# Kernel tuning notes

Measured on AMD Instinct MI355X. Metric: run time of the kernel, lower is better.

The kernel has to match this reference:

```python
import jax, jax.numpy as jnp
import numpy as np

N_HEADS = 16
DIM = 1024
HW = 32
B = 8


def _conv3x3(x, W, b):
    # x: [B, C, H, W], W: [O, I, 3, 3] (OIHW), padding 1 == SAME for stride 1
    y = jax.lax.conv_general_dilated(
        x, W, window_strides=(1, 1), padding='SAME',
        dimension_numbers=('NCHW', 'OIHW', 'NCHW'))
    return y + b[None, :, None, None]


def setup_inputs() -> dict:
    key = jax.random.key(0)
    ks = jax.random.split(key, 8)
    f32 = jnp.float32
    q = jax.random.normal(ks[0], (B, DIM, HW, HW), f32)
    k = jax.random.normal(ks[1], (B, DIM, HW, HW), f32)
    v = jax.random.normal(ks[2], (B, DIM, HW, HW), f32)
    Wq = jax.random.normal(ks[3], (DIM, DIM, 3, 3), f32) * 0.02
    Wk = jax.random.normal(ks[4], (DIM, DIM, 3, 3), f32) * 0.02
    Wv = jax.random.normal(ks[5], (DIM, DIM, 3, 3), f32) * 0.02
    Wo = jax.random.normal(ks[6], (DIM, DIM), f32) * 0.02
    bq = jnp.zeros((DIM,), f32); bk = jnp.zeros((DIM,), f32)
    bv = jnp.zeros((DIM,), f32); bo = jnp.zeros((DIM,), f32)
    mask = jax.random.randint(ks[7], (B, DIM, DIM), 0, 2, jnp.int32)
    return {'q': q, 'k': k, 'v': v, 'Wq': Wq, 'bq': bq, 'Wk': Wk, 'bk': bk,
            'Wv': Wv, 'bv': bv, 'Wo': Wo, 'bo': bo, 'mask': mask}


def reference(q, k, v, Wq, bq, Wk, bk, Wv, bv, Wo, bo, mask):
    Bq, C, H, W = q.shape  # C == dim, tokens = channels
    h = N_HEADS
    d = (H * W) // h  # head dim

    def split_heads(x):
        # [B, C, H, W] -> [B, h, C, d]
        return x.reshape(Bq, C, h, d).transpose(0, 2, 1, 3)

    qh = split_heads(_conv3x3(q, Wq, bq))
    kh = split_heads(_conv3x3(k, Wk, bk))
    vh = split_heads(_conv3x3(v, Wv, bv))

    scale = 1.0 / np.sqrt(d).astype(np.float32)
    attn = jnp.einsum('bhtd,bhsd->bhts', qh, kh) * scale  # [B, h, C, C]
    attn = jnp.where(mask[:, None, :, :] == 0, jnp.float32(-1e9), attn)
    w = jax.nn.softmax(attn, axis=-1)  # attn_dropout rate = 0 -> identity
    out = jnp.einsum('bhts,bhsd->bhtd', w, vh)  # [B, h, C, d]
    out = out.transpose(0, 2, 1, 3).reshape(Bq, C, h * d)  # [B, C, H*W]
    out = out @ Wo.T + bo  # Linear(dim, dim); H*W == dim
    return out
```

## Files before the change

### kernel.cpp

```cpp
#include <hip/hip_runtime.h>

typedef __attribute__((ext_vector_type(8))) short bh8;
typedef __attribute__((ext_vector_type(4))) short bh4;
typedef __attribute__((ext_vector_type(4))) float f32x4;

__device__ __forceinline__ short f2bf(float f) {
  union { float f; unsigned u; } a; a.f = f;
  unsigned r = a.u + 0x7FFFu + ((a.u >> 16) & 1u);
  return (short)(r >> 16);
}

__device__ __forceinline__ void g2l16(const short* g, short* l) {
  __builtin_amdgcn_global_load_lds(
      (const __attribute__((address_space(1))) void*)g,
      (__attribute__((address_space(3))) void*)l, 16, 0, 0);
}

__device__ __forceinline__ void barrier_raw() {
  asm volatile("" ::: "memory");
  __builtin_amdgcn_s_barrier();
  asm volatile("" ::: "memory");
}

__global__ __launch_bounds__(256) void zero_halo(short* __restrict__ xP) {
  int z = blockIdx.y;
  short* base = xP + (size_t)z * 1183744;
  int ri = blockIdx.x * 2 + (threadIdx.x >> 7);
  int row;
  if (ri < 34) row = ri;
  else if (ri < 68) row = 1122 + (ri - 34);
  else { int j = ri - 68; int y = (j >> 1) + 1; int x = (j & 1) ? 33 : 0; row = y * 34 + x; }
  int col = (threadIdx.x & 127) * 8;
  bh8 zv = {0, 0, 0, 0, 0, 0, 0, 0};
  *(bh8*)(base + (size_t)row * 1024 + col) = zv;
}

__global__ __launch_bounds__(256) void transpose3(
    const float* __restrict__ q, const float* __restrict__ k, const float* __restrict__ v,
    short* __restrict__ qP, short* __restrict__ kP, short* __restrict__ vP) {
  int z = blockIdx.z; int tensor = z >> 3, b = z & 7;
  const float* src = tensor == 0 ? q : (tensor == 1 ? k : v);
  short* dst = tensor == 0 ? qP : (tensor == 1 ? kP : vP);
  src += (size_t)b * 1048576; dst += (size_t)b * 1183744;
  int row0 = blockIdx.y * 64;
  int col0 = blockIdx.x * 64;
  __shared__ short t[64][72];
  int tid = threadIdx.x;
#pragma unroll
  for (int i = 0; i < 2; ++i) {
    int cid = tid + i * 256;
    int r = cid >> 3, co = (cid & 7) * 8;
    const float* p = src + (size_t)(row0 + r) * 1024 + col0 + co;
    float4 f0 = *(const float4*)(p);
    float4 f1 = *(const float4*)(p + 4);
    t[co + 0][r] = f2bf(f0.x); t[co + 1][r] = f2bf(f0.y);
    t[co + 2][r] = f2bf(f0.z); t[co + 3][r] = f2bf(f0.w);
    t[co + 4][r] = f2bf(f1.x); t[co + 5][r] = f2bf(f1.y);
    t[co + 6][r] = f2bf(f1.z); t[co + 7][r] = f2bf(f1.w);
  }
  __syncthreads();
#pragma unroll
  for (int i = 0; i < 2; ++i) {
    int cid = tid + i * 256;
    int sr = cid >> 3, cc = (cid & 7) * 8;
    bh8 val = *(const bh8*)&t[sr][cc];
    int tok = col0 + sr;
    int pr = ((tok >> 5) + 1) * 34 + (tok & 31) + 1;
    *(bh8*)(dst + (size_t)pr * 1024 + row0 + cc) = val;
  }
}

__global__ __launch_bounds__(256) void wperm3(
    const float* __restrict__ Wq, const float* __restrict__ Wk, const float* __restrict__ Wv,
    short* __restrict__ WpQ, short* __restrict__ WpK, short* __restrict__ WpV) {
  int z = blockIdx.y;
  const float* W = z == 0 ? Wq : (z == 1 ? Wk : Wv);
  short* Wp = z == 0 ? WpQ : (z == 1 ? WpK : WpV);
  int idx = blockIdx.x * 256 + threadIdx.x;
  const float* wsrc = W + (size_t)idx * 9;
#pragma unroll
  for (int t = 0; t < 9; ++t) Wp[(size_t)t * 1048576 + idx] = f2bf(wsrc[t]);
}

__global__ __launch_bounds__(256) void cvt_bf(const float* __restrict__ src,
                                              short* __restrict__ dst) {
  int idx = (blockIdx.x * 256 + threadIdx.x) * 4;
  float4 f = *(const float4*)(src + idx);
  bh4 o; o[0] = f2bf(f.x); o[1] = f2bf(f.y); o[2] = f2bf(f.z); o[3] = f2bf(f.w);
  *(bh4*)(dst + idx) = o;
}

__global__ __launch_bounds__(256) void mask_pack(const int* __restrict__ m,
                                                 unsigned* __restrict__ mp) {
  int idx = blockIdx.x * 256 + threadIdx.x;
  const int* src = m + (size_t)idx * 32;
  unsigned wv = 0;
#pragma unroll
  for (int j = 0; j < 32; j += 4) {
    int4 a = *(const int4*)(src + j);
    wv |= ((unsigned)(a.x & 1) << j) | ((unsigned)(a.y & 1) << (j + 1)) |
          ((unsigned)(a.z & 1) << (j + 2)) | ((unsigned)(a.w & 1) << (j + 3));
  }
  mp[idx] = wv;
}

__global__ __launch_bounds__(512, 4) void conv_gemm_td(
    const short* __restrict__ WpQ, const short* __restrict__ WpK, const short* __restrict__ WpV,
    const short* __restrict__ xPq, const short* __restrict__ xPk, const short* __restrict__ xPv,
    short* __restrict__ cQ, short* __restrict__ cK, short* __restrict__ cVT,
    const float* __restrict__ bq, const float* __restrict__ bk, const float* __restrict__ bv,
    int convSel) {
  __shared__ short lds[36864];
  int tid = threadIdx.x, lane = tid & 63, wid = tid >> 6;

  int fid = blockIdx.x + (blockIdx.y << 2) + ((int)blockIdx.z << 5);
  int nwg = (int)gridDim.z << 5;
  int cpx = nwg >> 3;
  int swz = (fid & 7) * cpx + (fid >> 3);
  int mtile = swz & 3, ntile = (swz >> 2) & 7, z = swz >> 5;

  int conv = convSel >= 0 ? convSel : (z >> 3);
  int b = convSel >= 0 ? z : (z & 7);
  const short* Wp = conv == 0 ? WpQ : (conv == 1 ? WpK : WpV);
  const short* xP = conv == 0 ? xPq : (conv == 1 ? xPk : xPv);
  short* out = conv == 0 ? cQ : (conv == 1 ? cK : cVT);
  const float* bias = conv == 0 ? bq : (conv == 1 ? bk : bv);
  int XisA = (conv == 2);
  int mbase = mtile * 256, nbase = ntile * 128;
  const short* xb = xP + (size_t)b * 1183744;

  int srow = tid >> 2;
  int lsl = (tid & 3) ^ ((tid >> 3) & 3);
  int gcol = lsl * 8;
  const short* pA0; const short* pA1; const short* pB0;
  if (!XisA) {
    pA0 = Wp + (size_t)(mbase + srow) * 1024 + gcol;
    pA1 = Wp + (size_t)(mbase + 128 + srow) * 1024 + gcol;
    int tok = nbase + srow;
    pB0 = xb + (size_t)(((tok >> 5) + 1) * 34 + (tok & 31) + 1) * 1024 + gcol;
  } else {
    int ta = mbase + srow, tb = mbase + 128 + srow;
    pA0 = xb + (size_t)(((ta >> 5) + 1) * 34 + (ta & 31) + 1) * 1024 + gcol;
    pA1 = xb + (size_t)(((tb >> 5) + 1) * 34 + (tb & 31) + 1) * 1024 + gcol;
    pB0 = Wp + (size_t)(nbase + srow) * 1024 + gcol;
  }
  int sdst = tid * 8;

  int pslot = (((lane >> 4) ^ ((lane >> 1) & 3)) << 3);
  int wr = wid >> 1, wc = wid & 1;
  int rdA = (wr * 64 + (lane & 15)) * 32 + pslot;
  int rdB = 8192 + (wc * 64 + (lane & 15)) * 32 + pslot;

  f32x4 acc[4][4] = {};

#define STAGE(U, SRB) do { \
    int u_ = (U); \
    int tap_ = u_ >> 5, kk_ = (u_ & 31) << 5; \
    int ty_ = (tap_ * 11) >> 5; \
    ptrdiff_t dW_ = (ptrdiff_t)tap_ * 1048576 + kk_; \
    ptrdiff_t dX_ = (ptrdiff_t)(ty_ * 34 + (tap_ - ty_ * 3) - 35) * 1024 + kk_; \
    ptrdiff_t dA_ = XisA ? dX_ : dW_, dB_ = XisA ? dW_ : dX_; \
    short* du_ = &lds[(SRB) + sdst]; \
    g2l16(pA0 + dA_, du_); \
    g2l16(pA1 + dA_, du_ + 4096); \
    g2l16(pB0 + dB_, du_ + 8192); \
  } while (0)

  STAGE(0, 0);
  STAGE(1, 12288);
  asm volatile("s_waitcnt vmcnt(3)" ::: "memory");
  barrier_raw();

#define TILEBODY(RB, T, DOSTAGE, SRB, WSTR) do { \
    const short* Lp = &lds[(RB)]; \
    bh8 afr[4], bfr[4]; \
    _Pragma("unroll") for (int mt = 0; mt < 4; ++mt) \
      afr[mt] = *(const bh8*)(Lp + rdA + mt * 512); \
    _Pragma("unroll") for (int nt = 0; nt < 4; ++nt) \
      bfr[nt] = *(const bh8*)(Lp + rdB + nt * 512); \
    if (DOSTAGE) STAGE((T) + 2, SRB); \
    __builtin_amdgcn_s_setprio(1); \
    _Pragma("unroll") for (int mt = 0; mt < 4; ++mt) { \
      _Pragma("unroll") for (int nt = 0; nt < 4; ++nt) \
        acc[mt][nt] = __builtin_amdgcn_mfma_f32_16x16x32_bf16( \
            afr[mt], bfr[nt], acc[mt][nt], 0, 0, 0); \
    } \
    __builtin_amdgcn_s_setprio(0); \
    asm volatile(WSTR ::: "memory"); \
    barrier_raw(); \
  } while (0)

#pragma unroll 1
  for (int it = 0; it < 95; ++it) {
    int t0 = it * 3;
    TILEBODY(0,     t0 + 0, true, 24576, "s_waitcnt vmcnt(3)");
    TILEBODY(12288, t0 + 1, true, 0,     "s_waitcnt vmcnt(3)");
    TILEBODY(24576, t0 + 2, true, 12288, "s_waitcnt vmcnt(3)");
  }
  TILEBODY(0,     285, true,  24576, "s_waitcnt vmcnt(3)");
  TILEBODY(12288, 286, false, 0,     "s_waitcnt vmcnt(0)");
  TILEBODY(24576, 287, false, 0,     "");

#undef TILEBODY
#undef STAGE

  size_t ob = (size_t)b * 1048576;
#pragma unroll
  for (int mt = 0; mt < 4; ++mt) {
#pragma unroll
    for (int nt = 0; nt < 4; ++nt) {
      int m0 = mbase + wr * 64 + mt * 16 + ((lane >> 4) << 2);
      int nn = nbase + wc * 64 + nt * 16 + (lane & 15);
#pragma unroll
      for (int r = 0; r < 4; ++r) {
        float bvv = bias[XisA ? nn : (m0 + r)];
        out[ob + (size_t)(m0 + r) * 1024 + nn] = f2bf(acc[mt][nt][r] + bvv);
      }
    }
  }
}

__global__ __launch_bounds__(256) void attn(
    const short* __restrict__ Qc, const short* __restrict__ Kc,
    const short* __restrict__ VT, const unsigned* __restrict__ Mp,
    short* __restrict__ AO) {
  __shared__ short sQ[64][72];
  __shared__ short sK[128][72];
  __shared__ short sV[64][136];
  __shared__ short sP[64][136];
  int tid = threadIdx.x, lane = tid & 63, w = tid >> 6;
  int qbase = blockIdx.x * 64, h = blockIdx.y, b = blockIdx.z;
  int j0 = h * 64;
  const short* Qb = Qc + (size_t)b * 1048576;
  const short* Kb = Kc + (size_t)b * 1048576;
  const short* Vb = VT + (size_t)b * 1048576;
  const unsigned* Mpb = Mp + (size_t)b * 32768;
  const float scale = 0.125f;

#pragma unroll
  for (int i = 0; i < 2; ++i) {
    int cid = tid + i * 256;
    int row = cid >> 3, co = (cid & 7) * 8;
    *(bh8*)&sQ[row][co] = *(const bh8*)(Qb + (size_t)(qbase + row) * 1024 + j0 + co);
  }
  __syncthreads();

  int tg = qbase + w * 16 + (lane & 15);
  int rsel = ((lane >> 4) << 2);
  float mrow = -3.0e38f, lrow = 0.0f;
  f32x4 oacc[4] = {};

  for (int st = 0; st < 8; ++st) {
#pragma unroll
    for (int i = 0; i < 4; ++i) {
      int cid = tid + i * 256;
      int row = cid >> 3, co = (cid & 7) * 8;
      *(bh8*)&sK[row][co] = *(const bh8*)(Kb + (size_t)(st * 128 + row) * 1024 + j0 + co);
      int vrow = cid >> 4, vco = (cid & 15) * 8;
      *(bh8*)&sV[vrow][vco] = *(const bh8*)(Vb + (size_t)(j0 + vrow) * 1024 + st * 128 + vco);
    }
    __syncthreads();

    f32x4 sacc[8];
#pragma unroll
    for (int mt = 0; mt < 8; ++mt) {
      f32x4 a = {0.f, 0.f, 0.f, 0.f};
      bh8 kf = *(const bh8*)&sK[mt * 16 + (lane & 15)][(lane >> 4) * 8];
      bh8 qf = *(const bh8*)&sQ[w * 16 + (lane & 15)][(lane >> 4) * 8];
      a = __builtin_amdgcn_mfma_f32_16x16x32_bf16(kf, qf, a, 0, 0, 0);
      kf = *(const bh8*)&sK[mt * 16 + (lane & 15)][32 + (lane >> 4) * 8];
      qf = *(const bh8*)&sQ[w * 16 + (lane & 15)][32 + (lane >> 4) * 8];
      a = __builtin_amdgcn_mfma_f32_16x16x32_bf16(kf, qf, a, 0, 0, 0);
      sacc[mt] = a;
    }

    uint4 Mw = *(const uint4*)(Mpb + (size_t)tg * 32 + st * 4);
    float tmax = -3.0e38f;
#pragma unroll
    for (int mt = 0; mt < 8; ++mt) {
      unsigned mwv = ((const unsigned*)&Mw)[mt >> 1] >> ((mt & 1) * 16 + rsel);
      f32x4 vv;
      vv[0] = (mwv & 1u) ? sacc[mt][0] * scale : -1e9f;
      vv[1] = (mwv & 2u) ? sacc[mt][1] * scale : -1e9f;
      vv[2] = (mwv & 4u) ? sacc[mt][2] * scale : -1e9f;
      vv[3] = (mwv & 8u) ? sacc[mt][3] * scale : -1e9f;
      sacc[mt] = vv;
      tmax = fmaxf(tmax, fmaxf(fmaxf(vv[0], vv[1]), fmaxf(vv[2], vv[3])));
    }
    tmax = fmaxf(tmax, __shfl_xor(tmax, 16, 64));
    tmax = fmaxf(tmax, __shfl_xor(tmax, 32, 64));
    float mnew = fmaxf(mrow, tmax);
    float alpha = __expf(fminf(mrow - mnew, 0.f));

    float sum = 0.f;
    uint4 Mw2 = Mw;
#pragma unroll
    for (int mt = 0; mt < 8; ++mt) {
      unsigned mwv = ((const unsigned*)&Mw2)[mt >> 1] >> ((mt & 1) * 16 + rsel);
      float p0 = (mwv & 1u) ? __expf(fminf(sacc[mt][0] - mnew, 0.f)) : 0.f;
      float p1 = (mwv & 2u) ? __expf(fminf(sacc[mt][1] - mnew, 0.f)) : 0.f;
      float p2 = (mwv & 4u) ? __expf(fminf(sacc[mt][2] - mnew, 0.f)) : 0.f;
      float p3 = (mwv & 8u) ? __expf(fminf(sacc[mt][3] - mnew, 0.f)) : 0.f;
      sum += (p0 + p1) + (p2 + p3);
      bh4 p; p[0] = f2bf(p0); p[1] = f2bf(p1); p[2] = f2bf(p2); p[3] = f2bf(p3);
      *(bh4*)&sP[w * 16 + (lane & 15)][mt * 16 + rsel] = p;
    }
    sum += __shfl_xor(sum, 16, 64);
    sum += __shfl_xor(sum, 32, 64);
    lrow = lrow * alpha + sum;
    mrow = mnew;

    float al[4];
#pragma unroll
    for (int r = 0; r < 4; ++r) al[r] = __shfl(alpha, rsel + r, 64);
#pragma unroll
    for (int nt = 0; nt < 4; ++nt)
#pragma unroll
      for (int r = 0; r < 4; ++r) oacc[nt][r] *= al[r];
    __syncthreads();

#pragma unroll
    for (int k0 = 0; k0 < 4; ++k0) {
      bh8 pf = *(const bh8*)&sP[w * 16 + (lane & 15)][k0 * 32 + (lane >> 4) * 8];
#pragma unroll
      for (int nt = 0; nt < 4; ++nt) {
        bh8 vf = *(const bh8*)&sV[nt * 16 + (lane & 15)][k0 * 32 + (lane >> 4) * 8];
        oacc[nt] = __builtin_amdgcn_mfma_f32_16x16x32_bf16(pf, vf, oacc[nt], 0, 0, 0);
      }
    }
    __syncthreads();
  }

  float rl[4];
#pragma unroll
  for (int r = 0; r < 4; ++r) rl[r] = 1.0f / __shfl(lrow, rsel + r, 64);
  size_t ob = (size_t)b * 1048576;
#pragma unroll
  for (int nt = 0; nt < 4; ++nt) {
    int j = nt * 16 + (lane & 15);
    int t0 = qbase + w * 16 + rsel;
#pragma unroll
    for (int r = 0; r < 4; ++r)
      AO[ob + (size_t)(t0 + r) * 1024 + j0 + j] = f2bf(oacc[nt][r] * rl[r]);
  }
}

__global__ __launch_bounds__(256) void gemm_bt(
    const short* __restrict__ A, const short* __restrict__ Bm,
    float* __restrict__ out, const float* __restrict__ bias) {
  __shared__ short sA[4096];
  __shared__ short sB[4096];
  int tid = threadIdx.x, lane = tid & 63, w = tid >> 6;
  int mbase = blockIdx.x * 128, nbase = blockIdx.y * 128;
  int colsh = (lane & 3) * 8;
  int ldsoff[2]; const short* ap[2]; const short* bp[2];
#pragma unroll
  for (int i = 0; i < 2; ++i) {
    int row = 32 * w + 16 * i + (lane >> 2);
    ldsoff[i] = (2 * w + i) * 512 + lane * 8;
    ap[i] = A + (size_t)(mbase + row) * 1024 + colsh;
    bp[i] = Bm + (size_t)(nbase + row) * 1024 + colsh;
  }
  f32x4 acc[4][4] = {};
  int wm = (w >> 1) * 64, wn = (w & 1) * 64;
  for (int kt = 0; kt < 1024; kt += 32) {
#pragma unroll
    for (int i = 0; i < 2; ++i) {
      g2l16(ap[i] + kt, sA + ldsoff[i]);
      g2l16(bp[i] + kt, sB + ldsoff[i]);
    }
    __syncthreads();
    bh8 af[4], bfr[4];
#pragma unroll
    for (int mt = 0; mt < 4; ++mt)
      af[mt] = *(const bh8*)&sA[(wm + mt * 16 + (lane & 15)) * 32 + (lane >> 4) * 8];
#pragma unroll
    for (int nt = 0; nt < 4; ++nt)
      bfr[nt] = *(const bh8*)&sB[(wn + nt * 16 + (lane & 15)) * 32 + (lane >> 4) * 8];
#pragma unroll
    for (int mt = 0; mt < 4; ++mt)
#pragma unroll
      for (int nt = 0; nt < 4; ++nt)
        acc[mt][nt] = __builtin_amdgcn_mfma_f32_16x16x32_bf16(af[mt], bfr[nt], acc[mt][nt], 0, 0, 0);
    __syncthreads();
  }
#pragma unroll
  for (int mt = 0; mt < 4; ++mt) {
#pragma unroll
    for (int nt = 0; nt < 4; ++nt) {
      int m0 = mbase + wm + mt * 16 + ((lane >> 4) << 2);
      int n = nbase + wn + nt * 16 + (lane & 15);
      float bv = bias[n];
#pragma unroll
      for (int r = 0; r < 4; ++r)
        out[(size_t)(m0 + r) * 1024 + n] = acc[mt][nt][r] + bv;
    }
  }
}

extern "C" void kernel_launch(void* const* d_in, const int* in_sizes, int n_in,
                              void* d_out, int out_size, void* d_ws, size_t ws_size,
                              hipStream_t stream) {
  (void)in_sizes; (void)n_in; (void)out_size;
  const float* q    = (const float*)d_in[0];
  const float* k    = (const float*)d_in[1];
  const float* v    = (const float*)d_in[2];
  const float* Wq   = (const float*)d_in[3];
  const float* bq   = (const float*)d_in[4];
  const float* Wk   = (const float*)d_in[5];
  const float* bk   = (const float*)d_in[6];
  const float* Wv   = (const float*)d_in[7];
  const float* bv   = (const float*)d_in[8];
  const float* Wo   = (const float*)d_in[9];
  const float* bo   = (const float*)d_in[10];
  const int*   mask = (const int*)d_in[11];
  float* out = (float*)d_out;
  char* ws = (char*)d_ws;

  const size_t XPE = 1156ull * 1024 * 8;
  const size_t XPB = XPE * 2;
  const size_t WPE = 9ull * 1048576;
  short* xPq = (short*)ws;
  short* xPk = xPq + XPE;
  short* xPv = xPk + XPE;
  short* WpQ = (short*)(ws + 3 * XPB);
  short* WpK = WpQ + WPE;
  short* WpV = WpK + WPE;
  char* p2 = ws + 3 * XPB + 3 * WPE * 2;

  bool fused = ws_size >= 167000000ull;
  short *cQ, *cK, *cVT, *WoB, *AO; unsigned* Mpk;
  if (fused) {
    cQ  = (short*)(p2);
    cK  = (short*)(p2 + 16777216);
    cVT = (short*)(p2 + 33554432);
    WoB = (short*)(p2 + 50331648);
    Mpk = (unsigned*)(p2 + 52428800);
    AO  = xPq;
  } else {
    cQ  = (short*)(p2);
    WoB = (short*)(p2 + 16777216);
    Mpk = (unsigned*)(p2 + 18874368);
    cK  = xPq;
    cVT = xPk;
    AO  = xPv;
  }

  zero_halo<<<dim3(66, 24), dim3(256), 0, stream>>>(xPq);
  transpose3<<<dim3(16, 16, 24), dim3(256), 0, stream>>>(q, k, v, xPq, xPk, xPv);
  wperm3<<<dim3(4096, 3), dim3(256), 0, stream>>>(Wq, Wk, Wv, WpQ, WpK, WpV);
  cvt_bf<<<dim3(1024), dim3(256), 0, stream>>>(Wo, WoB);
  mask_pack<<<dim3(1024), dim3(256), 0, stream>>>(mask, Mpk);
  if (fused) {
    conv_gemm_td<<<dim3(4, 8, 24), dim3(512), 0, stream>>>(
        WpQ, WpK, WpV, xPq, xPk, xPv, cQ, cK, cVT, bq, bk, bv, -1);
  } else {
    conv_gemm_td<<<dim3(4, 8, 8), dim3(512), 0, stream>>>(
        WpQ, WpK, WpV, xPq, xPk, xPv, cQ, cK, cVT, bq, bk, bv, 0);
    conv_gemm_td<<<dim3(4, 8, 8), dim3(512), 0, stream>>>(
        WpQ, WpK, WpV, xPq, xPk, xPv, cQ, cK, cVT, bq, bk, bv, 1);
    conv_gemm_td<<<dim3(4, 8, 8), dim3(512), 0, stream>>>(
        WpQ, WpK, WpV, xPq, xPk, xPv, cQ, cK, cVT, bq, bk, bv, 2);
  }
  attn<<<dim3(16, 16, 8), dim3(256), 0, stream>>>(cQ, cK, cVT, Mpk, AO);
  gemm_bt<<<dim3(64, 8), dim3(256), 0, stream>>>(AO, WoB, out, bo);
}
```

Measured before the change: 805.7 us.

## Double-buffer K tiles with async global-to-LDS loads and swizzled layout

The attention kernel now fills K and V shared tiles with global_load_lds direct copies instead of register-staged loads. K is double-buffered so the next step's K tile is fetched while the current one is used, and V is loaded asynchronously alongside the QK^T compute. Both tiles use an XOR-swizzled unpadded layout so fragment reads avoid bank conflicts. Barriers become raw s_barrier calls with explicit vmcnt waits, which relies on hand-counted outstanding-load numbers and adds ordering risk.

```diff
diff --git a/kernel.cpp b/kernel.cpp
--- a/kernel.cpp
+++ b/kernel.cpp
@@ -225,8 +225,8 @@
     const short* __restrict__ VT, const unsigned* __restrict__ Mp,
     short* __restrict__ AO) {
   __shared__ short sQ[64][72];
-  __shared__ short sK[128][72];
-  __shared__ short sV[64][136];
+  __shared__ short sK[2][8192];
+  __shared__ short sV[8192];
   __shared__ short sP[64][136];
   int tid = threadIdx.x, lane = tid & 63, w = tid >> 6;
   int qbase = blockIdx.x * 64, h = blockIdx.y, b = blockIdx.z;
@@ -243,32 +243,50 @@
     int row = cid >> 3, co = (cid & 7) * 8;
     *(bh8*)&sQ[row][co] = *(const bh8*)(Qb + (size_t)(qbase + row) * 1024 + j0 + co);
   }
+
+  const short* kSrc[4]; const short* vSrc[4]; int cDst[4];
+#pragma unroll
+  for (int i = 0; i < 4; ++i) {
+    int cid = tid + i * 256;
+    int lsl = (cid & 3) ^ ((cid >> 3) & 3);
+    int krow = (cid >> 2) & 127, khalf = cid >> 9;
+    kSrc[i] = Kb + (size_t)krow * 1024 + j0 + khalf * 32 + lsl * 8;
+    int vrow = (cid >> 2) & 63, vqtr = cid >> 8;
+    vSrc[i] = Vb + (size_t)(j0 + vrow) * 1024 + vqtr * 32 + lsl * 8;
+    cDst[i] = cid * 8;
+  }
+
+#pragma unroll
+  for (int i = 0; i < 4; ++i) g2l16(kSrc[i], &sK[0][cDst[i]]);
   __syncthreads();
 
   int tg = qbase + w * 16 + (lane & 15);
   int rsel = ((lane >> 4) << 2);
+  int ksel = (((lane >> 4) ^ ((lane >> 1) & 3)) << 3);
   float mrow = -3.0e38f, lrow = 0.0f;
   f32x4 oacc[4] = {};
 
   for (int st = 0; st < 8; ++st) {
-#pragma unroll
-    for (int i = 0; i < 4; ++i) {
-      int cid = tid + i * 256;
-      int row = cid >> 3, co = (cid & 7) * 8;
-      *(bh8*)&sK[row][co] = *(const bh8*)(Kb + (size_t)(st * 128 + row) * 1024 + j0 + co);
-      int vrow = cid >> 4, vco = (cid & 15) * 8;
-      *(bh8*)&sV[vrow][vco] = *(const bh8*)(Vb + (size_t)(j0 + vrow) * 1024 + st * 128 + vco);
-    }
-    __syncthreads();
-
+    if (st < 7) {
+      const short* ks = kSrc[0] + (size_t)(st + 1) * 131072;
+      short* kd = &sK[(st + 1) & 1][0];
+#pragma unroll
+      for (int i = 0; i < 4; ++i)
+        g2l16(kSrc[i] + (size_t)(st + 1) * 131072, kd + cDst[i]);
+      (void)ks;
+    }
+#pragma unroll
+    for (int i = 0; i < 4; ++i) g2l16(vSrc[i] + (size_t)st * 128, &sV[cDst[i]]);
+
+    const short* Kr = &sK[st & 1][0];
     f32x4 sacc[8];
 #pragma unroll
     for (int mt = 0; mt < 8; ++mt) {
       f32x4 a = {0.f, 0.f, 0.f, 0.f};
-      bh8 kf = *(const bh8*)&sK[mt * 16 + (lane & 15)][(lane >> 4) * 8];
+      bh8 kf = *(const bh8*)(Kr + (mt * 16 + (lane & 15)) * 32 + ksel);
       bh8 qf = *(const bh8*)&sQ[w * 16 + (lane & 15)][(lane >> 4) * 8];
       a = __builtin_amdgcn_mfma_f32_16x16x32_bf16(kf, qf, a, 0, 0, 0);
-      kf = *(const bh8*)&sK[mt * 16 + (lane & 15)][32 + (lane >> 4) * 8];
+      kf = *(const bh8*)(Kr + 4096 + (mt * 16 + (lane & 15)) * 32 + ksel);
       qf = *(const bh8*)&sQ[w * 16 + (lane & 15)][32 + (lane >> 4) * 8];
       a = __builtin_amdgcn_mfma_f32_16x16x32_bf16(kf, qf, a, 0, 0, 0);
       sacc[mt] = a;
@@ -293,10 +311,9 @@
     float alpha = __expf(fminf(mrow - mnew, 0.f));
 
     float sum = 0.f;
-    uint4 Mw2 = Mw;
 #pragma unroll
     for (int mt = 0; mt < 8; ++mt) {
-      unsigned mwv = ((const unsigned*)&Mw2)[mt >> 1] >> ((mt & 1) * 16 + rsel);
+      unsigned mwv = ((const unsigned*)&Mw)[mt >> 1] >> ((mt & 1) * 16 + rsel);
       float p0 = (mwv & 1u) ? __expf(fminf(sacc[mt][0] - mnew, 0.f)) : 0.f;
       float p1 = (mwv & 2u) ? __expf(fminf(sacc[mt][1] - mnew, 0.f)) : 0.f;
       float p2 = (mwv & 4u) ? __expf(fminf(sacc[mt][2] - mnew, 0.f)) : 0.f;
@@ -317,18 +334,23 @@
     for (int nt = 0; nt < 4; ++nt)
 #pragma unroll
       for (int r = 0; r < 4; ++r) oacc[nt][r] *= al[r];
-    __syncthreads();
+
+    if (st < 7) asm volatile("s_waitcnt vmcnt(4)" ::: "memory");
+    else        asm volatile("s_waitcnt vmcnt(0)" ::: "memory");
+    barrier_raw();
 
 #pragma unroll
     for (int k0 = 0; k0 < 4; ++k0) {
       bh8 pf = *(const bh8*)&sP[w * 16 + (lane & 15)][k0 * 32 + (lane >> 4) * 8];
 #pragma unroll
       for (int nt = 0; nt < 4; ++nt) {
-        bh8 vf = *(const bh8*)&sV[nt * 16 + (lane & 15)][k0 * 32 + (lane >> 4) * 8];
+        bh8 vf = *(const bh8*)(sV + k0 * 2048 + (nt * 16 + (lane & 15)) * 32 + ksel);
         oacc[nt] = __builtin_amdgcn_mfma_f32_16x16x32_bf16(pf, vf, oacc[nt], 0, 0, 0);
       }
     }
-    __syncthreads();
+
+    asm volatile("s_waitcnt vmcnt(0)" ::: "memory");
+    barrier_raw();
   }
 
   float rl[4];
```

After: 785.1 us. 1.03x faster.
